# Optimization experiments

Measured on AMD Instinct MI355X. Metric: run time of the kernel, lower is better.

## Reference

```python
import jax, jax.numpy as jnp
import numpy as np

N = 100000
E = 1600000
IN_C = 512
OUT_C = 128


def setup_inputs() -> dict:
    key = jax.random.key(0)
    k1, k2, k3, k4 = jax.random.split(key, 4)
    x = jax.random.normal(k1, (N, IN_C), dtype=jnp.float32)
    edge_index = jax.random.randint(k2, (2, E), 0, N, dtype=jnp.int64)
    # GCNConv parameters (glorot weight, zero bias as in PyG defaults)
    scale = jnp.sqrt(6.0 / (IN_C + OUT_C)).astype(jnp.float32)
    W = jax.random.uniform(k3, (IN_C, OUT_C), dtype=jnp.float32, minval=-scale, maxval=scale)
    b = jnp.zeros((OUT_C,), dtype=jnp.float32)
    return {"x": x, "edge_index": edge_index, "W": W, "b": b}


def reference(x, edge_index, W, b):
    n = x.shape[0]
    loops = jnp.arange(n, dtype=edge_index.dtype)
    src = jnp.concatenate([edge_index[0], loops])  # [E+N] message sources
    dst = jnp.concatenate([edge_index[1], loops])  # [E+N] message targets
    # symmetric GCN normalization: deg over targets incl. self-loops
    deg = jax.ops.segment_sum(jnp.ones_like(src, dtype=x.dtype), dst, num_segments=n)
    dinv = jnp.where(deg > 0, jax.lax.rsqrt(deg), 0.0)
    norm = dinv[src] * dinv[dst]  # [E+N]
    h = x @ W  # [N, OUT_C] transform first (in > out)
    msg = h[src] * norm[:, None]  # [E+N, OUT_C]
    out = jax.ops.segment_sum(msg, dst, num_segments=n) + b
    return (out, 0)
```

## Files before the change

### kernel.cpp

```cpp
#include <hip/hip_runtime.h>

#define IN_C 512
#define OUT_C 128
#define NB 128
#define CHUNK 8192

typedef float f32x4 __attribute__((ext_vector_type(4)));
typedef __bf16 bf16x8 __attribute__((ext_vector_type(8)));

static inline int cdiv(int a, int b) { return (a + b - 1) / b; }

__device__ __forceinline__ unsigned short bfbits(__bf16 h) {
  return __builtin_bit_cast(unsigned short, h);
}
__device__ __forceinline__ float bflo(unsigned int u) {
  return __builtin_bit_cast(float, u << 16);
}
__device__ __forceinline__ float bfhi(unsigned int u) {
  return __builtin_bit_cast(float, u & 0xffff0000u);
}

__global__ __launch_bounds__(256) void hist_kernel(const int* __restrict__ dst,
                                                   int* __restrict__ table,
                                                   const float* __restrict__ W,
                                                   unsigned short* __restrict__ wfh,
                                                   unsigned short* __restrict__ wfl,
                                                   int nchunks, int E) {
  int c = blockIdx.x;
  int t = threadIdx.x;
  if (c >= nchunks) {
    int i = (c - nchunks) * 256 + t;
    if (i < IN_C * OUT_C) {
      int k = i >> 7;
      int col = i & 127;
      float w = W[i];
      __bf16 hb = (__bf16)w;
      __bf16 lb = (__bf16)(w - (float)hb);
      int ks = k >> 5;
      int lg = (k & 31) >> 3;
      int j = k & 7;
      int cb = col >> 4;
      int lane = lg * 16 + (col & 15);
      size_t idx = ((size_t)(ks * 8 + cb) * 64 + lane) * 8 + j;
      wfh[idx] = bfbits(hb);
      wfl[idx] = bfbits(lb);
    }
    return;
  }
  __shared__ int hcnt[NB];
  if (t < NB) hcnt[t] = 0;
  __syncthreads();
  int base = c * CHUNK;
  int lim = base + CHUNK < E ? base + CHUNK : E;
  for (int e = base + t; e < lim; e += 256) {
    atomicAdd(&hcnt[dst[e] >> 10], 1);
  }
  __syncthreads();
  if (t < NB) table[t * nchunks + c] = hcnt[t];
}

__device__ __forceinline__ void gemm_tile(
    const float* __restrict__ x, const unsigned short* __restrict__ wfh,
    const unsigned short* __restrict__ wfl, unsigned short* __restrict__ h,
    int n, int tile) {
  __shared__ float xs[2][4096];

  const int tid = threadIdx.x;
  const int wv = tid >> 6;
  const int lane = tid & 63;
  const int l15 = lane & 15;
  const int lg = lane >> 4;
  const int wr = wv >> 1;
  const int wc = wv & 1;
  const int row0 = tile * 128;

  const float* gsrc[4];
#pragma unroll
  for (int i = 0; i < 4; i++) {
    int pslot = i * 256 + tid;
    int row = pslot >> 3;
    int q = pslot & 7;
    int s = q ^ (row & 7);
    int grow = row0 + row;
    if (grow > n - 1) grow = n - 1;
    gsrc[i] = x + (size_t)grow * IN_C + s * 4;
  }

  const unsigned short* bph = wfh + ((size_t)(wc * 4) * 64 + lane) * 8;
  const unsigned short* bpl = wfl + ((size_t)(wc * 4) * 64 + lane) * 8;

  f32x4 acc[4][4];
#pragma unroll
  for (int i = 0; i < 4; i++)
#pragma unroll
    for (int j = 0; j < 4; j++) acc[i][j] = (f32x4)0.0f;

#pragma unroll
  for (int i = 0; i < 4; i++) {
    char* lp = (char*)&xs[0][0] + i * 4096 + wv * 1024;
    __builtin_amdgcn_global_load_lds(
        (const __attribute__((address_space(1))) void*)gsrc[i],
        (__attribute__((address_space(3))) void*)lp, 16, 0, 0);
    gsrc[i] += 32;
  }
  __syncthreads();

  int cur = 0;
  for (int ks = 0; ks < 16; ks++) {
    if (ks < 15) {
#pragma unroll
      for (int i = 0; i < 4; i++) {
        char* lp = (char*)&xs[cur ^ 1][0] + i * 4096 + wv * 1024;
        __builtin_amdgcn_global_load_lds(
            (const __attribute__((address_space(1))) void*)gsrc[i],
            (__attribute__((address_space(3))) void*)lp, 16, 0, 0);
        gsrc[i] += 32;
      }
    }
    bf16x8 bh[4], bl[4];
#pragma unroll
    for (int nt = 0; nt < 4; nt++) {
      bh[nt] = __builtin_bit_cast(bf16x8, *(const uint4*)(bph + (size_t)ks * 4096 + nt * 512));
      bl[nt] = __builtin_bit_cast(bf16x8, *(const uint4*)(bpl + (size_t)ks * 4096 + nt * 512));
    }
    const float* bp = &xs[cur][0];
    bf16x8 ah[4];
#pragma unroll
    for (int rt = 0; rt < 4; rt++) {
      int row = wr * 64 + rt * 16 + l15;
      int r7 = row & 7;
      int s0 = (lg * 2) ^ r7;
      int s1 = (lg * 2 + 1) ^ r7;
      float4 f0 = *(const float4*)(bp + row * 32 + s0 * 4);
      float4 f1 = *(const float4*)(bp + row * 32 + s1 * 4);
      float f[8] = {f0.x, f0.y, f0.z, f0.w, f1.x, f1.y, f1.z, f1.w};
      bf16x8 hh;
#pragma unroll
      for (int j = 0; j < 8; j++) hh[j] = (__bf16)f[j];
      ah[rt] = hh;
    }
#pragma unroll
    for (int rt = 0; rt < 4; rt++)
#pragma unroll
      for (int nt = 0; nt < 4; nt++) {
        acc[rt][nt] = __builtin_amdgcn_mfma_f32_16x16x32_bf16(ah[rt], bh[nt], acc[rt][nt], 0, 0, 0);
        acc[rt][nt] = __builtin_amdgcn_mfma_f32_16x16x32_bf16(ah[rt], bl[nt], acc[rt][nt], 0, 0, 0);
      }
    __syncthreads();
    cur ^= 1;
  }

#pragma unroll
  for (int rt = 0; rt < 4; rt++) {
    int rowbase = row0 + wr * 64 + rt * 16 + lg * 4;
#pragma unroll
    for (int r = 0; r < 4; r++) {
      int row = rowbase + r;
      if (row < n) {
#pragma unroll
        for (int nt = 0; nt < 4; nt++) {
          int col = wc * 64 + nt * 16 + l15;
          h[(size_t)row * OUT_C + col] = bfbits((__bf16)acc[rt][nt][r]);
        }
      }
    }
  }
}

__global__ __launch_bounds__(256) void tscan_gemm_kernel(
    int* __restrict__ table, int* __restrict__ bstart,
    const float* __restrict__ x, const unsigned short* __restrict__ wfh,
    const unsigned short* __restrict__ wfl, unsigned short* __restrict__ h,
    int nchunks, int E, int n, int tbase) {
  if (blockIdx.x != 0) {
    gemm_tile(x, wfh, wfl, h, n, tbase + (int)blockIdx.x - 1);
    return;
  }
  __shared__ int sh[256];
  int t = threadIdx.x;
  int total = NB * nchunks;
  int S = (total + 255) / 256;
  int lo = t * S;
  int hi = lo + S; if (hi > total) hi = total;
  int s = 0;
  int i = lo;
  for (; i + 4 <= hi; i += 4)
    s += table[i] + table[i + 1] + table[i + 2] + table[i + 3];
  for (; i < hi; i++) s += table[i];
  sh[t] = s;
  __syncthreads();
  for (int off = 1; off < 256; off <<= 1) {
    int x2 = sh[t];
    if (t >= off) x2 += sh[t - off];
    __syncthreads();
    sh[t] = x2;
    __syncthreads();
  }
  int run = sh[t] - s;
  for (i = lo; i < hi; i++) {
    int v = table[i];
    table[i] = run;
    run += v;
  }
  __syncthreads();
  for (int b = t; b < NB; b += 256) bstart[b] = table[b * nchunks];
  if (t == 0) bstart[NB] = E;
}

__global__ __launch_bounds__(256) void scat2_gemm_kernel(
    const int* __restrict__ src, const int* __restrict__ dst,
    const int* __restrict__ table, int* __restrict__ inter,
    const float* __restrict__ x, const unsigned short* __restrict__ wfh,
    const unsigned short* __restrict__ wfl, unsigned short* __restrict__ h,
    int nchunks, int E, int n, int tbase) {
  if ((int)blockIdx.x >= nchunks) {
    gemm_tile(x, wfh, wfl, h, n, tbase + (int)blockIdx.x - nchunks);
    return;
  }
  __shared__ int cur[NB];
  int t = threadIdx.x;
  int c = blockIdx.x;
  if (t < NB) cur[t] = table[t * nchunks + c];
  __syncthreads();
  int base = c * CHUNK;
  int lim = base + CHUNK < E ? base + CHUNK : E;
  for (int e = base + t; e < lim; e += 256) {
    int d = dst[e];
    int pos = atomicAdd(&cur[d >> 10], 1);
    inter[pos] = (src[e] << 10) | (d & 1023);
  }
}

__global__ __launch_bounds__(256) void bucket_gemm_kernel(
    const int* __restrict__ inter, const int* __restrict__ bstart,
    int* __restrict__ offs, float* __restrict__ dinv, int* __restrict__ csr_src,
    const float* __restrict__ x, const unsigned short* __restrict__ wfh,
    const unsigned short* __restrict__ wfl, unsigned short* __restrict__ h,
    int n, int E, int nbk, int tbase) {
  if ((int)blockIdx.x >= nbk) {
    gemm_tile(x, wfh, wfl, h, n, tbase + (int)blockIdx.x - nbk);
    return;
  }
  __shared__ int dl[1024];
  __shared__ int curs[1024];
  __shared__ int sh[256];
  int t = threadIdx.x;
  int b = blockIdx.x;
  for (int i = t; i < 1024; i += 256) dl[i] = 0;
  __syncthreads();
  int lo = bstart[b], hi = bstart[b + 1];
  for (int e = lo + t; e < hi; e += 256) atomicAdd(&dl[inter[e] & 1023], 1);
  __syncthreads();
  int c[4];
  int s = 0;
#pragma unroll
  for (int j = 0; j < 4; j++) {
    c[j] = dl[t * 4 + j];
    s += c[j];
  }
  sh[t] = s;
  __syncthreads();
  for (int off = 1; off < 256; off <<= 1) {
    int x2 = sh[t];
    if (t >= off) x2 += sh[t - off];
    __syncthreads();
    sh[t] = x2;
    __syncthreads();
  }
  int run = sh[t] - s + lo;
  int nb0 = b << 10;
#pragma unroll
  for (int j = 0; j < 4; j++) {
    int node = nb0 + t * 4 + j;
    if (node < n) {
      offs[node] = run;
      dinv[node] = rsqrtf((float)c[j] + 1.0f);
    }
    curs[t * 4 + j] = run;
    run += c[j];
  }
  if (b == nbk - 1 && t == 255) offs[n] = E;
  __syncthreads();
  for (int e = lo + t; e < hi; e += 256) {
    int u = inter[e];
    int pos = atomicAdd(&curs[u & 1023], 1);
    csr_src[pos] = u >> 10;
  }
}

__global__ __launch_bounds__(256) void hscale_kernel(uint4* __restrict__ hw,
                                                     const float* __restrict__ dinv,
                                                     int n) {
  int gid = blockIdx.x * 256 + threadIdx.x;
  int total = n * 16;
  if (gid >= total) return;
  int row = gid >> 4;
  float d = dinv[row];
  uint4 u = hw[gid];
  auto sc = [&](unsigned int v) -> unsigned int {
    unsigned short lb = bfbits((__bf16)(bflo(v) * d));
    unsigned short hb = bfbits((__bf16)(bfhi(v) * d));
    return (unsigned int)lb | ((unsigned int)hb << 16);
  };
  u.x = sc(u.x); u.y = sc(u.y); u.z = sc(u.z); u.w = sc(u.w);
  hw[gid] = u;
}

__global__ __launch_bounds__(256) void gather_kernel(const int* __restrict__ offs,
                                                     const int* __restrict__ csr_src,
                                                     const unsigned short* __restrict__ h,
                                                     const float* __restrict__ dinv,
                                                     const float* __restrict__ b,
                                                     float* __restrict__ out,
                                                     int n, int tail) {
  int wid = threadIdx.x >> 6;
  int lane = threadIdx.x & 63;
  int l15 = lane & 15;
  int q = lane >> 4;
  int node = blockIdx.x * 4 + wid;
  if (node >= n) return;

  int start = offs[node];
  int end = offs[node + 1];

  float ax0 = 0, ay0 = 0, ax1 = 0, ay1 = 0, ax2 = 0, ay2 = 0, ax3 = 0, ay3 = 0;

  int e = start + q;
  for (; e + 12 < end; e += 16) {
    int s0 = csr_src[e];
    int s1 = csr_src[e + 4];
    int s2 = csr_src[e + 8];
    int s3 = csr_src[e + 12];
    uint4 u0 = *(const uint4*)(h + (size_t)s0 * OUT_C + l15 * 8);
    uint4 u1 = *(const uint4*)(h + (size_t)s1 * OUT_C + l15 * 8);
    uint4 u2 = *(const uint4*)(h + (size_t)s2 * OUT_C + l15 * 8);
    uint4 u3 = *(const uint4*)(h + (size_t)s3 * OUT_C + l15 * 8);
    ax0 += (bflo(u0.x) + bflo(u1.x)) + (bflo(u2.x) + bflo(u3.x));
    ay0 += (bfhi(u0.x) + bfhi(u1.x)) + (bfhi(u2.x) + bfhi(u3.x));
    ax1 += (bflo(u0.y) + bflo(u1.y)) + (bflo(u2.y) + bflo(u3.y));
    ay1 += (bfhi(u0.y) + bfhi(u1.y)) + (bfhi(u2.y) + bfhi(u3.y));
    ax2 += (bflo(u0.z) + bflo(u1.z)) + (bflo(u2.z) + bflo(u3.z));
    ay2 += (bfhi(u0.z) + bfhi(u1.z)) + (bfhi(u2.z) + bfhi(u3.z));
    ax3 += (bflo(u0.w) + bflo(u1.w)) + (bflo(u2.w) + bflo(u3.w));
    ay3 += (bfhi(u0.w) + bfhi(u1.w)) + (bfhi(u2.w) + bfhi(u3.w));
  }
  for (; e < end; e += 4) {
    int s0 = csr_src[e];
    uint4 u0 = *(const uint4*)(h + (size_t)s0 * OUT_C + l15 * 8);
    ax0 += bflo(u0.x); ay0 += bfhi(u0.x);
    ax1 += bflo(u0.y); ay1 += bfhi(u0.y);
    ax2 += bflo(u0.z); ay2 += bfhi(u0.z);
    ax3 += bflo(u0.w); ay3 += bfhi(u0.w);
  }

#pragma unroll
  for (int mask = 16; mask <= 32; mask <<= 1) {
    ax0 += __shfl_xor(ax0, mask); ay0 += __shfl_xor(ay0, mask);
    ax1 += __shfl_xor(ax1, mask); ay1 += __shfl_xor(ay1, mask);
    ax2 += __shfl_xor(ax2, mask); ay2 += __shfl_xor(ay2, mask);
    ax3 += __shfl_xor(ax3, mask); ay3 += __shfl_xor(ay3, mask);
  }

  float dd = dinv[node];
  uint4 us = *(const uint4*)(h + (size_t)node * OUT_C + l15 * 8);
  ax0 = (ax0 + bflo(us.x)) * dd; ay0 = (ay0 + bfhi(us.x)) * dd;
  ax1 = (ax1 + bflo(us.y)) * dd; ay1 = (ay1 + bfhi(us.y)) * dd;
  ax2 = (ax2 + bflo(us.z)) * dd; ay2 = (ay2 + bfhi(us.z)) * dd;
  ax3 = (ax3 + bflo(us.w)) * dd; ay3 = (ay3 + bfhi(us.w)) * dd;

  if (q == 0) {
    float4 b0 = *(const float4*)(b + l15 * 8);
    float4 b1 = *(const float4*)(b + l15 * 8 + 4);
    float4 o0 = make_float4(ax0 + b0.x, ay0 + b0.y, ax1 + b0.z, ay1 + b0.w);
    float4 o1 = make_float4(ax2 + b1.x, ay2 + b1.y, ax3 + b1.z, ay3 + b1.w);
    float* op = out + (size_t)node * OUT_C + l15 * 8;
    *(float4*)op = o0;
    *(float4*)(op + 4) = o1;
  }

  if (node == 0 && lane == 0) {
    for (int t = 0; t < tail; t++) out[(size_t)n * OUT_C + t] = 0.0f;
  }
}

extern "C" void kernel_launch(void* const* d_in, const int* in_sizes, int n_in,
                              void* d_out, int out_size, void* d_ws, size_t ws_size,
                              hipStream_t stream) {
  const float* x = (const float*)d_in[0];
  const int* ei = (const int*)d_in[1];
  const float* W = (const float*)d_in[2];
  const float* b = (const float*)d_in[3];

  const int n = in_sizes[0] / IN_C;
  const int E = in_sizes[1] / 2;
  const int* src = ei;
  const int* dst = ei + E;
  float* out = (float*)d_out;

  const int nchunks = cdiv(E, CHUNK);
  const int nbk = cdiv(n, 1024);
  const int ntiles = cdiv(n, 128);
  int t2 = ntiles < 128 ? ntiles : 128;
  int rem = ntiles - t2;
  int t3 = rem < 416 ? rem : 416;
  int t4 = rem - t3;

  size_t p = 0;
  auto alloc = [&](size_t bytes) { size_t o = p; p += (bytes + 255) & ~(size_t)255; return o; };
  char* ws = (char*)d_ws;
  float*          dinv   = (float*)(ws + alloc((size_t)n * 4));
  int*            offs   = (int*)(ws + alloc(((size_t)n + 1) * 4));
  int*            csrsrc = (int*)(ws + alloc((size_t)E * 4));
  int*            bstart = (int*)(ws + alloc((NB + 1) * 4));
  unsigned short* wfh    = (unsigned short*)(ws + alloc((size_t)IN_C * OUT_C * 2));
  unsigned short* wfl    = (unsigned short*)(ws + alloc((size_t)IN_C * OUT_C * 2));
  unsigned short* h      = (unsigned short*)(ws + alloc((size_t)n * OUT_C * 2));
  int*            inter  = (int*)(ws + alloc((size_t)E * 4));
  int*            table  = (int*)(ws + alloc((size_t)NB * nchunks * 4));

  hist_kernel<<<nchunks + 256, 256, 0, stream>>>(dst, table, W, wfh, wfl, nchunks, E);
  tscan_gemm_kernel<<<1 + t2, 256, 0, stream>>>(table, bstart, x, wfh, wfl, h,
                                                nchunks, E, n, 0);
  scat2_gemm_kernel<<<nchunks + t3, 256, 0, stream>>>(src, dst, table, inter,
                                                      x, wfh, wfl, h, nchunks, E, n, t2);
  bucket_gemm_kernel<<<nbk + t4, 256, 0, stream>>>(inter, bstart, offs, dinv, csrsrc,
                                                   x, wfh, wfl, h, n, E, nbk, t2 + t3);
  hscale_kernel<<<cdiv(n * 16, 256), 256, 0, stream>>>((uint4*)h, dinv, n);
  int tail = out_size - n * OUT_C;
  gather_kernel<<<cdiv(n, 4), 256, 0, stream>>>(offs, csrsrc, h, dinv, b, out, n, tail);
}
```

Measured before the change: 243.3 us.

## Split bucket scatter from degree pass and fuse it with h scaling

The final CSR scatter moves out of the bucket/degree kernel into a new kernel that also does the dinv row scaling of h. The two independent jobs now share one launch, and the degree kernel's tail GEMM tiles no longer wait behind the scatter. The chunk size is halved to give more histogram and scatter blocks, and the GEMM tiles are spread differently across the fused launches. The cost is that per-chunk table entries grow, and the scatter blocks must re-read the offsets from global memory.

```diff
diff --git a/kernel.cpp b/kernel.cpp
--- a/kernel.cpp
+++ b/kernel.cpp
@@ -3,7 +3,7 @@
 #define IN_C 512
 #define OUT_C 128
 #define NB 128
-#define CHUNK 8192
+#define CHUNK 4096
 
 typedef float f32x4 __attribute__((ext_vector_type(4)));
 typedef __bf16 bf16x8 __attribute__((ext_vector_type(8)));
@@ -231,9 +231,9 @@
   }
 }
 
-__global__ __launch_bounds__(256) void bucket_gemm_kernel(
+__global__ __launch_bounds__(256) void bdeg_gemm_kernel(
     const int* __restrict__ inter, const int* __restrict__ bstart,
-    int* __restrict__ offs, float* __restrict__ dinv, int* __restrict__ csr_src,
+    int* __restrict__ offs, float* __restrict__ dinv,
     const float* __restrict__ x, const unsigned short* __restrict__ wfh,
     const unsigned short* __restrict__ wfl, unsigned short* __restrict__ h,
     int n, int E, int nbk, int tbase) {
@@ -242,7 +242,6 @@
     return;
   }
   __shared__ int dl[1024];
-  __shared__ int curs[1024];
   __shared__ int sh[256];
   int t = threadIdx.x;
   int b = blockIdx.x;
@@ -276,34 +275,47 @@
       offs[node] = run;
       dinv[node] = rsqrtf((float)c[j] + 1.0f);
     }
-    curs[t * 4 + j] = run;
     run += c[j];
   }
   if (b == nbk - 1 && t == 255) offs[n] = E;
-  __syncthreads();
+}
+
+__global__ __launch_bounds__(256) void scat3_hscale_kernel(
+    const int* __restrict__ inter, const int* __restrict__ bstart,
+    const int* __restrict__ offs, int* __restrict__ csr_src,
+    uint4* __restrict__ hw, const float* __restrict__ dinv,
+    int n, int nbk) {
+  int t = threadIdx.x;
+  if ((int)blockIdx.x >= nbk) {
+    int gid = ((int)blockIdx.x - nbk) * 256 + t;
+    int total = n * 16;
+    if (gid >= total) return;
+    int row = gid >> 4;
+    float d = dinv[row];
+    uint4 u = hw[gid];
+    auto sc = [&](unsigned int v) -> unsigned int {
+      unsigned short lb = bfbits((__bf16)(bflo(v) * d));
+      unsigned short hb = bfbits((__bf16)(bfhi(v) * d));
+      return (unsigned int)lb | ((unsigned int)hb << 16);
+    };
+    u.x = sc(u.x); u.y = sc(u.y); u.z = sc(u.z); u.w = sc(u.w);
+    hw[gid] = u;
+    return;
+  }
+  __shared__ int curs[1024];
+  int b = blockIdx.x;
+  int nb0 = b << 10;
+  for (int i = t; i < 1024; i += 256) {
+    int node = nb0 + i;
+    curs[i] = (node < n) ? offs[node] : 0;
+  }
+  __syncthreads();
+  int lo = bstart[b], hi = bstart[b + 1];
   for (int e = lo + t; e < hi; e += 256) {
     int u = inter[e];
     int pos = atomicAdd(&curs[u & 1023], 1);
     csr_src[pos] = u >> 10;
   }
-}
-
-__global__ __launch_bounds__(256) void hscale_kernel(uint4* __restrict__ hw,
-                                                     const float* __restrict__ dinv,
-                                                     int n) {
-  int gid = blockIdx.x * 256 + threadIdx.x;
-  int total = n * 16;
-  if (gid >= total) return;
-  int row = gid >> 4;
-  float d = dinv[row];
-  uint4 u = hw[gid];
-  auto sc = [&](unsigned int v) -> unsigned int {
-    unsigned short lb = bfbits((__bf16)(bflo(v) * d));
-    unsigned short hb = bfbits((__bf16)(bfhi(v) * d));
-    return (unsigned int)lb | ((unsigned int)hb << 16);
-  };
-  u.x = sc(u.x); u.y = sc(u.y); u.z = sc(u.z); u.w = sc(u.w);
-  hw[gid] = u;
 }
 
 __global__ __launch_bounds__(256) void gather_kernel(const int* __restrict__ offs,
@@ -400,10 +412,11 @@
   const int nchunks = cdiv(E, CHUNK);
   const int nbk = cdiv(n, 1024);
   const int ntiles = cdiv(n, 128);
-  int t2 = ntiles < 128 ? ntiles : 128;
+  int t2 = ntiles < 255 ? ntiles : 255;
   int rem = ntiles - t2;
-  int t3 = rem < 416 ? rem : 416;
+  int t3 = rem < 400 ? rem : 400;
   int t4 = rem - t3;
+  const int nhs = cdiv(n * 16, 256);
 
   size_t p = 0;
   auto alloc = [&](size_t bytes) { size_t o = p; p += (bytes + 255) & ~(size_t)255; return o; };
@@ -423,9 +436,10 @@
                                                 nchunks, E, n, 0);
   scat2_gemm_kernel<<<nchunks + t3, 256, 0, stream>>>(src, dst, table, inter,
                                                       x, wfh, wfl, h, nchunks, E, n, t2);
-  bucket_gemm_kernel<<<nbk + t4, 256, 0, stream>>>(inter, bstart, offs, dinv, csrsrc,
-                                                   x, wfh, wfl, h, n, E, nbk, t2 + t3);
-  hscale_kernel<<<cdiv(n * 16, 256), 256, 0, stream>>>((uint4*)h, dinv, n);
+  bdeg_gemm_kernel<<<nbk + t4, 256, 0, stream>>>(inter, bstart, offs, dinv,
+                                                 x, wfh, wfl, h, n, E, nbk, t2 + t3);
+  scat3_hscale_kernel<<<nbk + nhs, 256, 0, stream>>>(inter, bstart, offs, csrsrc,
+                                                     (uint4*)h, dinv, n, nbk);
   int tail = out_size - n * OUT_C;
   gather_kernel<<<cdiv(n, 4), 256, 0, stream>>>(offs, csrsrc, h, dinv, b, out, n, tail);
 }
```

Measured after the change: 271.2 us. 11.5% more time.
